# Kernel optimization log

Hardware: AMD Instinct MI355X
Metric: run time of the kernel (lower is better)

The kernel has to match this reference:

```python
import jax, jax.numpy as jnp
import numpy as np

TOP_K = 2

def setup_inputs() -> dict:
    key = jax.random.key(0)
    k1, k2 = jax.random.split(key)
    x = jax.random.normal(k1, (8, 4096, 4096), dtype=jnp.float32)
    # nn.Linear weight [num_experts, dim]
    gate_w = jax.random.normal(k2, (64, 4096), dtype=jnp.float32) * (1.0 / np.sqrt(4096))
    return {"x": x, "gate_w": gate_w}

def reference(x, gate_w):
    # logits: [B, S, E]
    logits = jnp.einsum('bsd,ed->bse', x, gate_w)
    routing_weights = jax.nn.softmax(logits, axis=-1)
    top_weights, top_indices = jax.lax.top_k(routing_weights, TOP_K)
    top_weights = top_weights / jnp.sum(top_weights, axis=-1, keepdims=True)
    return top_weights, top_indices
```

## Files before the change

kernel.cpp:

```cpp
#include <hip/hip_runtime.h>
#include <hip/hip_bf16.h>
#include <math.h>


typedef __attribute__((ext_vector_type(8))) short short8;
typedef __attribute__((ext_vector_type(4))) float f32x4;

#define TPB 32
#define NCH 128
#define TAU 1e-4f
#define LROW 68

__device__ __forceinline__ void cvt8(const f32x4* v, short8* hi, short8* lo) {
    const float* f = reinterpret_cast<const float*>(v);
#pragma unroll
    for (int j = 0; j < 8; ++j) {
        __hip_bfloat16 h = __float2bfloat16(f[j]);
        float r = f[j] - __bfloat162float(h);
        __hip_bfloat16 l = __float2bfloat16(r);
        (*hi)[j] = (short)*reinterpret_cast<unsigned short*>(&h);
        (*lo)[j] = (short)*reinterpret_cast<unsigned short*>(&l);
    }
}

__global__ void prep_b(const float* __restrict__ gw,
                       short8* __restrict__ bh, short8* __restrict__ bl) {
    const int tid = blockIdx.x * 256 + threadIdx.x;
    const int ln  = tid & 63;
    const int w   = (tid >> 6) & 127;
    const int nt  = tid >> 13;
    const int row = nt * 16 + (ln & 15);
    const int k   = w * 32 + ((ln >> 4) << 3);
    f32x4 v[2];
    v[0] = *reinterpret_cast<const f32x4*>(gw + (long)row * 4096 + k);
    v[1] = *reinterpret_cast<const f32x4*>(gw + (long)row * 4096 + k + 4);
    short8 h, l;
    cvt8(v, &h, &l);
    bh[tid] = h;
    bl[tid] = l;
}

__device__ __forceinline__ void gload16(const void* g, void* l) {
    __builtin_amdgcn_global_load_lds(
        (const __attribute__((address_space(1))) void*)g,
        (__attribute__((address_space(3))) void*)l, 16, 0, 0);
}

#define STAGE(C, BUF) do {                                                    \
    char* aB = AB + (BUF) * 4096;                                             \
    char* bB = AB + 8192 + (BUF) * 8192;                                      \
    gload16(srcA + (long)(C) * 128, aB + wv * 1024 + ln * 16);                \
    gload16(bhp + (long)wv * 8192 + (C) * 64 + ln, bB + (wv * 2 + 0) * 1024 + ln * 16); \
    gload16(blp + (long)wv * 8192 + (C) * 64 + ln, bB + (wv * 2 + 1) * 1024 + ln * 16); \
} while (0)

__global__ __launch_bounds__(256, 4)
void router_fused(const float* __restrict__ x,
                  const short8* __restrict__ bhp,
                  const short8* __restrict__ blp,
                  const float* __restrict__ gw,
                  float* __restrict__ out,
                  int M, int K) {
    __shared__ __align__(16) char AB[24576];
    __shared__ int flags[TPB];
    __shared__ double Ld4[4][64];

    const int t  = threadIdx.x;
    const int wv = t >> 6;
    const int ln = t & 63;
    const int fr = ln & 15;
    const int q  = ln >> 4;
    const int mm = wv >> 1;
    const int nn = wv & 1;
    const long tok0 = (long)blockIdx.x * TPB;

    const int arow = wv * 8 + (ln >> 3);
    const int sw   = (ln & 7) ^ (ln >> 3);
    const char* srcA = (const char*)(x + (tok0 + arow) * (long)K) + sw * 16;

    f32x4 acc[2];
    acc[0] = (f32x4){0.f, 0.f, 0.f, 0.f};
    acc[1] = (f32x4){0.f, 0.f, 0.f, 0.f};

    STAGE(0, 0);
    STAGE(1, 1);

    for (int c = 0; c < NCH; ++c) {
        const int buf = c & 1;
        if (c + 1 < NCH) asm volatile("s_waitcnt vmcnt(3)" ::: "memory");
        else             asm volatile("s_waitcnt vmcnt(0)" ::: "memory");
        __builtin_amdgcn_s_barrier();
        asm volatile("" ::: "memory");
        __builtin_amdgcn_sched_barrier(0);

        {
            const char* aB = AB + buf * 4096;
            const char* bB = AB + 8192 + buf * 8192;
            const int r = mm * 16 + fr;
            f32x4 av[2];
            av[0] = *(const f32x4*)(aB + r * 128 + (((q * 2 + 0) ^ (fr & 7)) * 16));
            av[1] = *(const f32x4*)(aB + r * 128 + (((q * 2 + 1) ^ (fr & 7)) * 16));
            short8 ah, al;
            cvt8(av, &ah, &al);
#pragma unroll
            for (int ntl = 0; ntl < 2; ++ntl) {
                const int nt = 2 * nn + ntl;
                short8 bhv = *(const short8*)(bB + (nt * 2 + 0) * 1024 + ln * 16);
                short8 blv = *(const short8*)(bB + (nt * 2 + 1) * 1024 + ln * 16);
                acc[ntl] = __builtin_amdgcn_mfma_f32_16x16x32_bf16(ah, bhv, acc[ntl], 0, 0, 0);
                acc[ntl] = __builtin_amdgcn_mfma_f32_16x16x32_bf16(ah, blv, acc[ntl], 0, 0, 0);
                acc[ntl] = __builtin_amdgcn_mfma_f32_16x16x32_bf16(al, bhv, acc[ntl], 0, 0, 0);
                acc[ntl] = __builtin_amdgcn_mfma_f32_16x16x32_bf16(al, blv, acc[ntl], 0, 0, 0);
            }
        }

        __builtin_amdgcn_sched_barrier(0);
        asm volatile("" ::: "memory");
        __builtin_amdgcn_s_barrier();
        asm volatile("" ::: "memory");
        if (c + 2 < NCH) STAGE(c + 2, buf);
        __builtin_amdgcn_sched_barrier(0);
    }

    __syncthreads();
    float* Ls = (float*)AB;
#pragma unroll
    for (int ntl = 0; ntl < 2; ++ntl)
#pragma unroll
        for (int r = 0; r < 4; ++r)
            Ls[(mm * 16 + q * 4 + r) * LROW + (2 * nn + ntl) * 16 + fr] = acc[ntl][r];
    __syncthreads();

    if (t < TPB) {
        const float* row = Ls + (long)t * LROW;
        float m1 = -INFINITY, m2 = -INFINITY, m3 = -INFINITY;
        int i1 = 0, i2 = 0;
#pragma unroll 8
        for (int e = 0; e < 64; ++e) {
            const float v = row[e];
            if (v > m1)      { m3 = m2; m2 = m1; i2 = i1; m1 = v; i1 = e; }
            else if (v > m2) { m3 = m2; m2 = v; i2 = e; }
            else if (v > m3) { m3 = v; }
        }
        const float e2 = expf(m2 - m1);
        const float s  = 1.0f + e2;

        const long g = tok0 + t;
        out[2 * g + 0] = 1.0f / s;
        out[2 * g + 1] = e2 / s;
        float* oi = out + 2 * (long)M;
        oi[2 * g + 0] = (float)i1;
        oi[2 * g + 1] = (float)i2;

        flags[t] = ((m1 - m2) < TAU) | ((m2 - m3) < TAU);
    }
    __syncthreads();

    for (int tk = 0; tk < TPB; ++tk) {
        if (flags[tk]) {
            const float* xr = x + (tok0 + tk) * (long)K + wv * 1024;
            const float* gr = gw + (long)ln * (long)K + wv * 1024;
            double s0 = 0.0, s1 = 0.0, s2 = 0.0, s3 = 0.0;
            for (int k = 0; k < 1024; k += 4) {
                const f32x4 a = *reinterpret_cast<const f32x4*>(xr + k);
                const f32x4 b = *reinterpret_cast<const f32x4*>(gr + k);
                s0 = fma((double)a.x, (double)b.x, s0);
                s1 = fma((double)a.y, (double)b.y, s1);
                s2 = fma((double)a.z, (double)b.z, s2);
                s3 = fma((double)a.w, (double)b.w, s3);
            }
            Ld4[wv][ln] = (s0 + s1) + (s2 + s3);
            __syncthreads();
            if (t == 0) {
                double m1 = -INFINITY, m2 = -INFINITY;
                int i1 = 0, i2 = 0;
                for (int e = 0; e < 64; ++e) {
                    const double v = Ld4[0][e] + Ld4[1][e] + Ld4[2][e] + Ld4[3][e];
                    if (v > m1)      { m2 = m1; i2 = i1; m1 = v; i1 = e; }
                    else if (v > m2) { m2 = v; i2 = e; }
                }
                const double e2 = exp(m2 - m1);
                const double s  = 1.0 + e2;
                const long g = tok0 + tk;
                out[2 * g + 0] = (float)(1.0 / s);
                out[2 * g + 1] = (float)(e2 / s);
                float* oi = out + 2 * (long)M;
                oi[2 * g + 0] = (float)i1;
                oi[2 * g + 1] = (float)i2;
            }
            __syncthreads();
        }
    }
}

extern "C" void kernel_launch(void* const* d_in, const int* in_sizes, int n_in,
                              void* d_out, int out_size, void* d_ws, size_t ws_size,
                              hipStream_t stream) {
    const float* x  = (const float*)d_in[0];
    const float* gw = (const float*)d_in[1];
    float* out = (float*)d_out;

    const int K = 4096;
    const int M = in_sizes[0] / K;
    const int nblocks = M / TPB;

    short8* bh = (short8*)d_ws;
    short8* bl = bh + 32768;

    prep_b<<<128, 256, 0, stream>>>(gw, bh, bl);
    router_fused<<<nblocks, 256, 0, stream>>>(x, bh, bl, gw, out, M, K);
}
```

Before: 236.3 us.

## Stage wider A chunks in LDS and read gate weights directly from global

Each pipeline stage now loads 128 K-elements of the token rows into LDS instead of 32, so the loop runs 32 iterations instead of 128 and needs four times fewer barrier pairs. The pre-split bf16 hi/lo gate-weight fragments are no longer staged through LDS; each wave reads them straight from global memory, where they should stay cache-resident. The LDS swizzle is widened to fit the larger rows. The risk is that the in-loop global B loads share the vmcnt counter with the async A prefetch, so the waits needed for B may also stall on the next stage's A loads and weaken the overlap.

```diff
diff --git a/kernel.cpp b/kernel.cpp
--- a/kernel.cpp
+++ b/kernel.cpp
@@ -7,7 +7,7 @@
 typedef __attribute__((ext_vector_type(4))) float f32x4;
 
 #define TPB 32
-#define NCH 128
+#define NCH 32
 #define TAU 1e-4f
 #define LROW 68
 
@@ -47,11 +47,10 @@
 }
 
 #define STAGE(C, BUF) do {                                                    \
-    char* aB = AB + (BUF) * 4096;                                             \
-    char* bB = AB + 8192 + (BUF) * 8192;                                      \
-    gload16(srcA + (long)(C) * 128, aB + wv * 1024 + ln * 16);                \
-    gload16(bhp + (long)wv * 8192 + (C) * 64 + ln, bB + (wv * 2 + 0) * 1024 + ln * 16); \
-    gload16(blp + (long)wv * 8192 + (C) * 64 + ln, bB + (wv * 2 + 1) * 1024 + ln * 16); \
+    char* aB = AB + (BUF) * 16384;                                            \
+    _Pragma("unroll")                                                         \
+    for (int i = 0; i < 4; ++i)                                               \
+        gload16(srcA[i] + (long)(C) * 512, aB + (wv * 4 + i) * 1024 + ln * 16); \
 } while (0)
 
 __global__ __launch_bounds__(256, 4)
@@ -61,7 +60,7 @@
                   const float* __restrict__ gw,
                   float* __restrict__ out,
                   int M, int K) {
-    __shared__ __align__(16) char AB[24576];
+    __shared__ __align__(16) char AB[32768];
     __shared__ int flags[TPB];
     __shared__ double Ld4[4][64];
 
@@ -74,9 +73,14 @@
     const int nn = wv & 1;
     const long tok0 = (long)blockIdx.x * TPB;
 
-    const int arow = wv * 8 + (ln >> 3);
-    const int sw   = (ln & 7) ^ (ln >> 3);
-    const char* srcA = (const char*)(x + (tok0 + arow) * (long)K) + sw * 16;
+    const char* srcA[4];
+#pragma unroll
+    for (int i = 0; i < 4; ++i) {
+        const int row  = 2 * (wv * 4 + i) + (ln >> 5);
+        const int slot = (ln & 31);
+        const int swz  = (slot & ~7) | ((slot & 7) ^ (row & 7));
+        srcA[i] = (const char*)x + (tok0 + row) * (long)K * 4 + swz * 16;
+    }
 
     f32x4 acc[2];
     acc[0] = (f32x4){0.f, 0.f, 0.f, 0.f};
@@ -85,32 +89,37 @@
     STAGE(0, 0);
     STAGE(1, 1);
 
+    const int R = mm * 16 + fr;
+    const int rk = R & 7;
+
     for (int c = 0; c < NCH; ++c) {
         const int buf = c & 1;
-        if (c + 1 < NCH) asm volatile("s_waitcnt vmcnt(3)" ::: "memory");
+        if (c + 1 < NCH) asm volatile("s_waitcnt vmcnt(4)" ::: "memory");
         else             asm volatile("s_waitcnt vmcnt(0)" ::: "memory");
         __builtin_amdgcn_s_barrier();
         asm volatile("" ::: "memory");
         __builtin_amdgcn_sched_barrier(0);
 
         {
-            const char* aB = AB + buf * 4096;
-            const char* bB = AB + 8192 + buf * 8192;
-            const int r = mm * 16 + fr;
-            f32x4 av[2];
-            av[0] = *(const f32x4*)(aB + r * 128 + (((q * 2 + 0) ^ (fr & 7)) * 16));
-            av[1] = *(const f32x4*)(aB + r * 128 + (((q * 2 + 1) ^ (fr & 7)) * 16));
-            short8 ah, al;
-            cvt8(av, &ah, &al);
-#pragma unroll
-            for (int ntl = 0; ntl < 2; ++ntl) {
-                const int nt = 2 * nn + ntl;
-                short8 bhv = *(const short8*)(bB + (nt * 2 + 0) * 1024 + ln * 16);
-                short8 blv = *(const short8*)(bB + (nt * 2 + 1) * 1024 + ln * 16);
-                acc[ntl] = __builtin_amdgcn_mfma_f32_16x16x32_bf16(ah, bhv, acc[ntl], 0, 0, 0);
-                acc[ntl] = __builtin_amdgcn_mfma_f32_16x16x32_bf16(ah, blv, acc[ntl], 0, 0, 0);
-                acc[ntl] = __builtin_amdgcn_mfma_f32_16x16x32_bf16(al, bhv, acc[ntl], 0, 0, 0);
-                acc[ntl] = __builtin_amdgcn_mfma_f32_16x16x32_bf16(al, blv, acc[ntl], 0, 0, 0);
+            const char* aB = AB + buf * 16384 + R * 512;
+#pragma unroll
+            for (int w = 0; w < 4; ++w) {
+                f32x4 av[2];
+                av[0] = *(const f32x4*)(aB + (w * 8 + ((q * 2 + 0) ^ rk)) * 16);
+                av[1] = *(const f32x4*)(aB + (w * 8 + ((q * 2 + 1) ^ rk)) * 16);
+                short8 ah, al;
+                cvt8(av, &ah, &al);
+                const int widx = c * 4 + w;
+#pragma unroll
+                for (int ntl = 0; ntl < 2; ++ntl) {
+                    const int nt = 2 * nn + ntl;
+                    short8 bhv = bhp[nt * 8192 + widx * 64 + ln];
+                    short8 blv = blp[nt * 8192 + widx * 64 + ln];
+                    acc[ntl] = __builtin_amdgcn_mfma_f32_16x16x32_bf16(ah, bhv, acc[ntl], 0, 0, 0);
+                    acc[ntl] = __builtin_amdgcn_mfma_f32_16x16x32_bf16(ah, blv, acc[ntl], 0, 0, 0);
+                    acc[ntl] = __builtin_amdgcn_mfma_f32_16x16x32_bf16(al, bhv, acc[ntl], 0, 0, 0);
+                    acc[ntl] = __builtin_amdgcn_mfma_f32_16x16x32_bf16(al, blv, acc[ntl], 0, 0, 0);
+                }
             }
         }
 
```

Measured after the change: 247.2 us. 1.05x slower.
